# Kernel tuning notes

Measured on AMD Instinct MI355X. Metric: run time of the kernel, lower is better.

Reference implementation:

```python
import jax, jax.numpy as jnp
from jax import lax
import numpy as np

B, S, D = 64, 512, 256
VOCAB, NC = 50000, 10
N_STEPS = 10  # ode_step=11 points -> 10 intervals, h=0.1
BN_EPS = 1e-5


def setup_inputs() -> dict:
    key = jax.random.key(0)
    ks = jax.random.split(key, 16)
    inp = {}
    inp['input_ids'] = jax.random.randint(ks[0], (B, S), 0, VOCAB)
    inp['emb'] = jax.random.normal(ks[1], (VOCAB, D), dtype=jnp.float32)
    inp['W_ode'] = 0.1 * jax.random.normal(ks[2], (D, D), dtype=jnp.float32)  # init std=0.1
    inp['b_ode'] = jnp.zeros((D,), dtype=jnp.float32)
    for i, kk in enumerate([3, 4, 5]):
        fan_in = D * kk
        inp[f'w{kk}'] = jax.random.normal(ks[3 + 3 * i], (128, D, kk), jnp.float32) / np.sqrt(fan_in)
        inp[f'b{kk}'] = jax.random.normal(ks[4 + 3 * i], (128,), jnp.float32) * 0.01
        inp[f'g{kk}'] = jnp.ones((128,), jnp.float32)
        inp[f'be{kk}'] = jnp.zeros((128,), jnp.float32)
    inp['wc'] = jax.random.normal(ks[12], (NC, D + 3 * 128), jnp.float32) / np.sqrt(D + 3 * 128)
    inp['bc'] = jnp.zeros((NC,), jnp.float32)
    return inp


def _forward(input_ids, emb, W_ode, b_ode, w3, b3, g3, be3, w4, b4, g4, be4,
             w5, b5, g5, be5, wc, bc):
    x = emb[input_ids]                      # (B,S,D)
    # --- Neural ODE branch: linear RHS f(z) = z W^T + b, RK4 fixed-step on [0,1] ---
    z0 = x.reshape(-1, D)                   # (B*S, D)
    h = jnp.float32(1.0 / N_STEPS)

    def f(z):
        return z @ W_ode.T + b_ode

    def step(z, _):
        k1 = f(z)
        k2 = f(z + 0.5 * h * k1)
        k3 = f(z + 0.5 * h * k2)
        k4 = f(z + h * k3)
        return z + (h / 6.0) * (k1 + 2 * k2 + 2 * k3 + k4), None

    z, _ = lax.scan(step, z0, None, length=N_STEPS)
    node_pooled = z.reshape(B, S, D).max(axis=1)   # global max over seq -> (B,D)

    # --- TextCNN branches on raw embeddings ---
    cin = jnp.transpose(x, (0, 2, 1))       # (B,D,S)
    inv_std = jnp.float32(1.0 / np.sqrt(1.0 + BN_EPS))  # BN eval: mean=0, var=1

    def branch(w, b, g, be):
        c = lax.conv_general_dilated(cin, w, (1,), 'VALID',
                                     dimension_numbers=('NCH', 'OIH', 'NCH'))
        c = c + b[None, :, None]
        c = g[None, :, None] * (c * inv_std) + be[None, :, None]
        c = jax.nn.relu(c)
        return c.max(axis=2)                # (B,128)

    p3 = branch(w3, b3, g3, be3)
    p4 = branch(w4, b4, g4, be4)
    p5 = branch(w5, b5, g5, be5)

    feats = jnp.concatenate([node_pooled, p3, p4, p5], axis=1)  # (B,640)
    return feats @ wc.T + bc                # (B,NC); dropout is identity in eval


def reference(input_ids, emb, W_ode, b_ode, w3, b3, g3, be3, w4, b4, g4, be4,
              w5, b5, g5, be5, wc, bc):
    return _forward(input_ids, emb, W_ode, b_ode, w3, b3, g3, be3,
                    w4, b4, g4, be4, w5, b5, g5, be5, wc, bc)
```

## Files before the change

kernel.cpp:

```cpp
#include <hip/hip_runtime.h>


typedef short bf16x8 __attribute__((ext_vector_type(8)));
typedef float f32x4 __attribute__((ext_vector_type(4)));

__device__ __forceinline__ unsigned short f2bf(float f) {
  unsigned u = __float_as_uint(f);
  u += 0x7FFFu + ((u >> 16) & 1u);
  return (unsigned short)(u >> 16);
}

__device__ __forceinline__ float dotcol64(const float* __restrict__ xrow,
                                          const float* __restrict__ Y, int c) {
  float a0 = 0.f, a1 = 0.f, a2 = 0.f, a3 = 0.f;
#pragma unroll 1
  for (int w = 0; w < 4; ++w) {
    float bv[64];
#pragma unroll
    for (int v = 0; v < 64; ++v) bv[v] = Y[(w * 64 + v) * 256 + c];
#pragma unroll
    for (int v = 0; v < 64; v += 4) {
      a0 = fmaf(xrow[w * 64 + v + 0], bv[v + 0], a0);
      a1 = fmaf(xrow[w * 64 + v + 1], bv[v + 1], a1);
      a2 = fmaf(xrow[w * 64 + v + 2], bv[v + 2], a2);
      a3 = fmaf(xrow[w * 64 + v + 3], bv[v + 3], a3);
    }
  }
  return (a0 + a1) + (a2 + a3);
}

__global__ __launch_bounds__(256) void k_prep1(
    const float* __restrict__ W, const float* __restrict__ bode,
    const float* __restrict__ w3c, const float* __restrict__ w4c, const float* __restrict__ w5c,
    float* __restrict__ Bm, float* __restrict__ c1,
    unsigned short* __restrict__ slab, unsigned* __restrict__ featbuf) {
  __shared__ float r1[256], r2[256], r3[256], red[4];
  const int tid = threadIdx.x, blk = blockIdx.x;
  if (blk < 256) {
    const int i = blk;
    r1[tid] = W[i * 256 + tid];
    __syncthreads();
    const float v2 = dotcol64(r1, W, tid);
    r2[tid] = v2;
    __syncthreads();
    const float v3 = dotcol64(r2, W, tid);
    r3[tid] = v3;
    __syncthreads();
    const float v4 = dotcol64(r3, W, tid);
    const float w1 = r1[tid];
    Bm[i * 256 + tid] = 0.1f * w1 + 0.005f * v2
                      + (0.001f / 6.f) * v3 + (0.0001f / 24.f) * v4;
    const float q = 0.05f * w1 + (0.01f / 6.f) * v2 + (0.001f / 24.f) * v3;
    float val = bode[tid] * q;
#pragma unroll
    for (int off = 32; off > 0; off >>= 1) val += __shfl_down(val, off);
    if ((tid & 63) == 0) red[tid >> 6] = val;
    __syncthreads();
    if (tid == 0) c1[i] = 0.1f * (bode[i] + ((red[0] + red[1]) + (red[2] + red[3])));
  } else {
    const int base = (blk - 256) * 256 + tid;
#pragma unroll
    for (int u = 0; u < 4; ++u) {
      int e = base + u * 98304;
      int s = e >> 15, r = e & 32767;
      int o = r >> 8, kd = r & 255;
      const float* w; int k, j;
      if (s < 3)      { w = w3c; k = 3; j = s; }
      else if (s < 7) { w = w4c; k = 4; j = s - 3; }
      else            { w = w5c; k = 5; j = s - 7; }
      float val = w[(o * 256 + kd) * k + j];
      int kc = kd >> 5, quad = (kd >> 3) & 3, q8 = kd & 7;
      slab[s * 32768 + ((kc * 4 + quad) * 128 + o) * 8 + q8] = f2bf(val);
    }
    if (base < 64 * 640) featbuf[base] = 0u;
  }
}

__global__ __launch_bounds__(256) void k_prep2a(
    const float* __restrict__ Bm, const float* __restrict__ c1v,
    float* __restrict__ Dm, float* __restrict__ c1b) {
  __shared__ float r1[256], c1s[256], red[4];
  const int tid = threadIdx.x, i = blockIdx.x;
  r1[tid] = Bm[i * 256 + tid];
  c1s[tid] = c1v[tid];
  __syncthreads();
  const float v2 = dotcol64(r1, Bm, tid);
  Dm[i * 256 + tid] = 2.f * r1[tid] + v2;
  float pd = r1[tid] * c1s[tid];
#pragma unroll
  for (int off = 32; off > 0; off >>= 1) pd += __shfl_down(pd, off);
  if ((tid & 63) == 0) red[tid >> 6] = pd;
  __syncthreads();
  if (tid == 0) c1b[i] = 2.f * c1s[i] + ((red[0] + red[1]) + (red[2] + red[3]));
}

__global__ __launch_bounds__(256) void k_prep2b(
    const float* __restrict__ Dm, const float* __restrict__ c1bv,
    float* __restrict__ c10, unsigned short* __restrict__ slab) {
  __shared__ float curs[256], cbs[256], red[4];
  const int tid = threadIdx.x, i = blockIdx.x;
  const float coefN[6] = {1.f, 5.f, 10.f, 10.f, 5.f, 1.f};
  const float coefC[5] = {5.f, 10.f, 10.f, 5.f, 1.f};
  float v = Dm[i * 256 + tid];
  curs[tid] = v;
  cbs[tid] = c1bv[tid];
  __syncthreads();
  float n10 = ((i == tid) ? 1.f : 0.f) + coefN[1] * v;
  float pd = v * cbs[tid];
#pragma unroll
  for (int off = 32; off > 0; off >>= 1) pd += __shfl_down(pd, off);
  if ((tid & 63) == 0) red[tid >> 6] = pd;
  __syncthreads();
  float ct = coefC[0] * cbs[i] + coefC[1] * ((red[0] + red[1]) + (red[2] + red[3]));

#pragma unroll 1
  for (int k = 2; k <= 5; ++k) {
    v = dotcol64(curs, Dm, tid);
    __syncthreads();
    curs[tid] = v;
    n10 = fmaf(coefN[k], v, n10);
    float pdk = v * cbs[tid];
#pragma unroll
    for (int off = 32; off > 0; off >>= 1) pdk += __shfl_down(pdk, off);
    if ((tid & 63) == 0) red[tid >> 6] = pdk;
    __syncthreads();
    if (k <= 4) ct = fmaf(coefC[k], (red[0] + red[1]) + (red[2] + red[3]), ct);
  }

  {
    const int o = i, kd = tid;
    const int kc = kd >> 5, quad = (kd >> 3) & 3, q8 = kd & 7;
    slab[(12 + (o >> 7)) * 32768 + ((kc * 4 + quad) * 128 + (o & 127)) * 8 + q8] = f2bf(n10);
  }
  if (tid == 0) c10[i] = ct;
}


__global__ __launch_bounds__(256, 4) void k_main(
    const int* __restrict__ ids, const float* __restrict__ emb,
    const unsigned short* __restrict__ slab, const float* __restrict__ ctot,
    const float* __restrict__ b3, const float* __restrict__ g3, const float* __restrict__ be3,
    const float* __restrict__ b4, const float* __restrict__ g4, const float* __restrict__ be4,
    const float* __restrict__ b5, const float* __restrict__ g5, const float* __restrict__ be5,
    unsigned* __restrict__ featbuf) {
  __shared__ alignas(16) unsigned short Xt[36 * 264];
  __shared__ int ids_s[36];
  const int tid = threadIdx.x;
  const int blk = blockIdx.x;
  const int b = blk & 63;
  const int t0 = (blk >> 6) * 32;
  const int lane = tid & 63;
  const int wave = tid >> 6;
  const int m15 = lane & 15;
  const int quad = lane >> 4;

  if (tid < 36) {
    int t = t0 + tid;
    ids_s[tid] = (t < 512) ? ids[b * 512 + t] : -1;
  }
  __syncthreads();
  for (int i = tid; i < 36 * 64; i += 256) {
    int row = i >> 6, s4 = i & 63;
    uint2 v = make_uint2(0u, 0u);
    int id = ids_s[row];
    if (id >= 0) {
      const float4 f = *(const float4*)(emb + (size_t)id * 256 + s4 * 4);
      v.x = (unsigned)f2bf(f.x) | ((unsigned)f2bf(f.y) << 16);
      v.y = (unsigned)f2bf(f.z) | ((unsigned)f2bf(f.w) << 16);
    }
    *(uint2*)&Xt[row * 264 + s4 * 4] = v;
  }
  __syncthreads();

  const unsigned short* fb0 = slab + ((size_t)quad * 128 + (wave * 2 + 0) * 16 + m15) * 8;
  const unsigned short* fb1 = fb0 + 128;

  bf16x8 fA[4], fB[4];
#pragma unroll
  for (int q = 0; q < 4; ++q) {
    fA[q] = *(const bf16x8*)(((q & 1) ? fb1 : fb0) + (q >> 1) * 4096);
    fB[q] = *(const bf16x8*)(((q & 1) ? fb1 : fb0) + 8192 + (q >> 1) * 4096);
  }

  f32x4 acc[2][2];
#pragma unroll
  for (int mt = 0; mt < 2; ++mt)
#pragma unroll
    for (int nt = 0; nt < 2; ++nt) acc[mt][nt] = (f32x4){0.f, 0.f, 0.f, 0.f};

#define ENTRY(KCQ, FR)                                                          \
  {                                                                             \
    __builtin_amdgcn_s_setprio(1);                                              \
    _Pragma("unroll")                                                           \
    for (int kc2 = 0; kc2 < 2; ++kc2) {                                         \
      const int kd0 = ((KCQ) * 2 + kc2) * 32 + quad * 8;                        \
      bf16x8 af[2];                                                             \
      _Pragma("unroll")                                                         \
      for (int mt = 0; mt < 2; ++mt)                                            \
        af[mt] = *(const bf16x8*)&Xt[(shift + mt * 16 + m15) * 264 + kd0];      \
      _Pragma("unroll")                                                         \
      for (int mt = 0; mt < 2; ++mt) {                                          \
        acc[mt][0] = __builtin_amdgcn_mfma_f32_16x16x32_bf16(af[mt], FR[kc2 * 2 + 0], acc[mt][0], 0, 0, 0); \
        acc[mt][1] = __builtin_amdgcn_mfma_f32_16x16x32_bf16(af[mt], FR[kc2 * 2 + 1], acc[mt][1], 0, 0, 0); \
      }                                                                         \
    }                                                                           \
    __builtin_amdgcn_s_setprio(0);                                              \
  }

  for (int ep = 0; ep < 28; ++ep) {
    const int e0 = ep * 2;
    const int slice = e0 >> 2;
    const int shift = (slice < 3) ? slice
                    : (slice < 7) ? (slice - 3)
                    : (slice < 12) ? (slice - 7) : 0;
    const int kcq0 = e0 & 3;

    ENTRY(kcq0, fA);
    if (ep < 27) {
      const int eo = (e0 + 2) * 8192;
#pragma unroll
      for (int q = 0; q < 4; ++q)
        fA[q] = *(const bf16x8*)(((q & 1) ? fb1 : fb0) + eo + (q >> 1) * 4096);
    }
    ENTRY(kcq0 + 1, fB);
    if (ep < 27) {
      const int eo = (e0 + 3) * 8192;
#pragma unroll
      for (int q = 0; q < 4; ++q)
        fB[q] = *(const bf16x8*)(((q & 1) ? fb1 : fb0) + eo + (q >> 1) * 4096);
    }

    const int g = (ep == 5) ? 0 : (ep == 13) ? 1 : (ep == 23) ? 2
                : (ep == 25) ? 3 : (ep == 27) ? 4 : -1;
    if (g >= 0) {
      if (g < 3) {
        const int kk = g + 3;
        const float* bb  = (g == 0) ? b3 : (g == 1) ? b4 : b5;
        const float* gg  = (g == 0) ? g3 : (g == 1) ? g4 : g5;
        const float* bbe = (g == 0) ? be3 : (g == 1) ? be4 : be5;
        const int off = 256 + g * 128;
        const int tmax = 512 - kk;
#pragma unroll
        for (int nt = 0; nt < 2; ++nt) {
          const int n = (wave * 2 + nt) * 16 + m15;
          const float sc = gg[n] * 0.9999950000375f;
          const float sh = fmaf(sc, bb[n], bbe[n]);
          float mx = 0.f;
#pragma unroll
          for (int mt = 0; mt < 2; ++mt)
#pragma unroll
            for (int r = 0; r < 4; ++r) {
              const int t = t0 + mt * 16 + quad * 4 + r;
              const float v = fmaf(sc, acc[mt][nt][r], sh);
              if (t <= tmax) mx = fmaxf(mx, v);
            }
          mx = fmaxf(mx, __shfl_xor(mx, 16));
          mx = fmaxf(mx, __shfl_xor(mx, 32));
          if (quad == 0) atomicMax(&featbuf[b * 640 + off + n], __float_as_uint(mx));
        }
      } else {
        const int base = (g == 3) ? 0 : 128;
#pragma unroll
        for (int nt = 0; nt < 2; ++nt) {
          const int n = (wave * 2 + nt) * 16 + m15;
          const float ct = ctot[base + n];
          float mx = -3.4e38f;
#pragma unroll
          for (int mt = 0; mt < 2; ++mt)
#pragma unroll
            for (int r = 0; r < 4; ++r)
              mx = fmaxf(mx, acc[mt][nt][r] + ct);
          mx = fmaxf(mx, __shfl_xor(mx, 16));
          mx = fmaxf(mx, __shfl_xor(mx, 32));
          if (quad == 0) {
            unsigned bits = __float_as_uint(mx);
            unsigned key = (bits & 0x80000000u) ? ~bits : (bits | 0x80000000u);
            atomicMax(&featbuf[b * 640 + base + n], key);
          }
        }
      }
#pragma unroll
      for (int mt = 0; mt < 2; ++mt)
#pragma unroll
        for (int nt = 0; nt < 2; ++nt) acc[mt][nt] = (f32x4){0.f, 0.f, 0.f, 0.f};
    }
  }
#undef ENTRY
}

__global__ void k_fin(const unsigned* __restrict__ featbuf, const float* __restrict__ wc,
                      const float* __restrict__ bc, float* __restrict__ out) {
  int b = blockIdx.x, lane = threadIdx.x;
  float p[10];
#pragma unroll
  for (int c = 0; c < 10; ++c) p[c] = 0.f;
  for (int f = lane; f < 640; f += 64) {
    unsigned u = featbuf[b * 640 + f];
    float v;
    if (f < 256) v = (u & 0x80000000u) ? __uint_as_float(u ^ 0x80000000u) : __uint_as_float(~u);
    else v = __uint_as_float(u);
#pragma unroll
    for (int c = 0; c < 10; ++c) p[c] = fmaf(v, wc[c * 640 + f], p[c]);
  }
#pragma unroll
  for (int c = 0; c < 10; ++c) {
    float s = p[c];
#pragma unroll
    for (int off = 32; off > 0; off >>= 1) s += __shfl_down(s, off);
    if (lane == 0) out[b * 10 + c] = s + bc[c];
  }
}

extern "C" void kernel_launch(void* const* d_in, const int* in_sizes, int n_in,
                              void* d_out, int out_size, void* d_ws, size_t ws_size,
                              hipStream_t stream) {
  (void)in_sizes; (void)n_in; (void)out_size; (void)ws_size;
  const int*   ids  = (const int*)d_in[0];
  const float* emb  = (const float*)d_in[1];
  const float* W    = (const float*)d_in[2];
  const float* bode = (const float*)d_in[3];
  const float* w3   = (const float*)d_in[4];
  const float* b3   = (const float*)d_in[5];
  const float* g3   = (const float*)d_in[6];
  const float* be3  = (const float*)d_in[7];
  const float* w4   = (const float*)d_in[8];
  const float* b4   = (const float*)d_in[9];
  const float* g4   = (const float*)d_in[10];
  const float* be4  = (const float*)d_in[11];
  const float* w5   = (const float*)d_in[12];
  const float* b5   = (const float*)d_in[13];
  const float* g5   = (const float*)d_in[14];
  const float* be5  = (const float*)d_in[15];
  const float* wc   = (const float*)d_in[16];
  const float* bc   = (const float*)d_in[17];
  float* out = (float*)d_out;

  float* wsf = (float*)d_ws;
  float* Bm  = wsf;
  float* Dm  = wsf + 65536;
  float* c1  = wsf + 131072;
  float* c1b = wsf + 131328;
  float* c10 = wsf + 131584;
  unsigned short* slab = (unsigned short*)(wsf + 131840);
  unsigned* featbuf = (unsigned*)(wsf + 361216);

  hipLaunchKernelGGL(k_prep1, dim3(640), dim3(256), 0, stream,
                     W, bode, w3, w4, w5, Bm, c1, slab, featbuf);
  hipLaunchKernelGGL(k_prep2a, dim3(256), dim3(256), 0, stream, Bm, c1, Dm, c1b);
  hipLaunchKernelGGL(k_prep2b, dim3(256), dim3(256), 0, stream, Dm, c1b, c10, slab);
  hipLaunchKernelGGL(k_main, dim3(1024), dim3(256), 0, stream,
                     ids, emb, slab, c10,
                     b3, g3, be3, b4, g4, be4, b5, g5, be5, featbuf);
  hipLaunchKernelGGL(k_fin, dim3(64), dim3(64), 0, stream, featbuf, wc, bc, out);
}
```

Measured before the change: 202.7 us.

## Fuse ODE matrix-power prep into main kernel with flag-based overlap

The k_prep2b kernel is folded into k_main. The first 256 blocks compute the RK4 propagator power and bias, store them with agent-scope atomics, and bump a completion counter. The conv blocks wait on that counter only before the ODE slabs at epoch 23, so the prep work overlaps the conv work and one launch is removed. Each main block now covers 64 timesteps instead of 32, which halves the block count and doubles accumulator tiles per wave, and setprio is dropped. The spin-wait relies on the producer blocks being scheduled first; if they are not, the kernel can deadlock. The larger tiles also raise register and LDS pressure.

```diff
diff --git a/kernel.cpp b/kernel.cpp
--- a/kernel.cpp
+++ b/kernel.cpp
@@ -8,6 +8,13 @@
   unsigned u = __float_as_uint(f);
   u += 0x7FFFu + ((u >> 16) & 1u);
   return (unsigned short)(u >> 16);
+}
+
+__device__ __forceinline__ void gstf(float* p, float v) {
+  __hip_atomic_store(p, v, __ATOMIC_RELAXED, __HIP_MEMORY_SCOPE_AGENT);
+}
+__device__ __forceinline__ void gst16(unsigned short* p, unsigned short v) {
+  __hip_atomic_store(p, v, __ATOMIC_RELAXED, __HIP_MEMORY_SCOPE_AGENT);
 }
 
 __device__ __forceinline__ float dotcol64(const float* __restrict__ xrow,
@@ -72,7 +79,7 @@
       int kc = kd >> 5, quad = (kd >> 3) & 3, q8 = kd & 7;
       slab[s * 32768 + ((kc * 4 + quad) * 128 + o) * 8 + q8] = f2bf(val);
     }
-    if (base < 64 * 640) featbuf[base] = 0u;
+    if (base <= 64 * 640) featbuf[base] = 0u;
   }
 }
 
@@ -94,72 +101,81 @@
   if (tid == 0) c1b[i] = 2.f * c1s[i] + ((red[0] + red[1]) + (red[2] + red[3]));
 }
 
-__global__ __launch_bounds__(256) void k_prep2b(
-    const float* __restrict__ Dm, const float* __restrict__ c1bv,
-    float* __restrict__ c10, unsigned short* __restrict__ slab) {
-  __shared__ float curs[256], cbs[256], red[4];
-  const int tid = threadIdx.x, i = blockIdx.x;
-  const float coefN[6] = {1.f, 5.f, 10.f, 10.f, 5.f, 1.f};
-  const float coefC[5] = {5.f, 10.f, 10.f, 5.f, 1.f};
-  float v = Dm[i * 256 + tid];
-  curs[tid] = v;
-  cbs[tid] = c1bv[tid];
-  __syncthreads();
-  float n10 = ((i == tid) ? 1.f : 0.f) + coefN[1] * v;
-  float pd = v * cbs[tid];
-#pragma unroll
-  for (int off = 32; off > 0; off >>= 1) pd += __shfl_down(pd, off);
-  if ((tid & 63) == 0) red[tid >> 6] = pd;
-  __syncthreads();
-  float ct = coefC[0] * cbs[i] + coefC[1] * ((red[0] + red[1]) + (red[2] + red[3]));
-
-#pragma unroll 1
-  for (int k = 2; k <= 5; ++k) {
-    v = dotcol64(curs, Dm, tid);
-    __syncthreads();
-    curs[tid] = v;
-    n10 = fmaf(coefN[k], v, n10);
-    float pdk = v * cbs[tid];
-#pragma unroll
-    for (int off = 32; off > 0; off >>= 1) pdk += __shfl_down(pdk, off);
-    if ((tid & 63) == 0) red[tid >> 6] = pdk;
-    __syncthreads();
-    if (k <= 4) ct = fmaf(coefC[k], (red[0] + red[1]) + (red[2] + red[3]), ct);
-  }
-
-  {
-    const int o = i, kd = tid;
-    const int kc = kd >> 5, quad = (kd >> 3) & 3, q8 = kd & 7;
-    slab[(12 + (o >> 7)) * 32768 + ((kc * 4 + quad) * 128 + (o & 127)) * 8 + q8] = f2bf(n10);
-  }
-  if (tid == 0) c10[i] = ct;
-}
-
 
 __global__ __launch_bounds__(256, 4) void k_main(
     const int* __restrict__ ids, const float* __restrict__ emb,
-    const unsigned short* __restrict__ slab, const float* __restrict__ ctot,
+    unsigned short* __restrict__ slab, const float* __restrict__ Dm,
+    const float* __restrict__ c1bv, float* __restrict__ c10,
     const float* __restrict__ b3, const float* __restrict__ g3, const float* __restrict__ be3,
     const float* __restrict__ b4, const float* __restrict__ g4, const float* __restrict__ be4,
     const float* __restrict__ b5, const float* __restrict__ g5, const float* __restrict__ be5,
     unsigned* __restrict__ featbuf) {
-  __shared__ alignas(16) unsigned short Xt[36 * 264];
-  __shared__ int ids_s[36];
+  __shared__ alignas(16) unsigned short Xt[68 * 264];
+  __shared__ int ids_s[68];
   const int tid = threadIdx.x;
   const int blk = blockIdx.x;
-  const int b = blk & 63;
-  const int t0 = (blk >> 6) * 32;
+  unsigned* nodecnt = featbuf + 64 * 640;
+
+  if (blk < 256) {
+    float* curs = (float*)Xt;
+    float* cbs  = curs + 256;
+    float* redp = curs + 512;
+    const int i = blk;
+    const float coefN[6] = {1.f, 5.f, 10.f, 10.f, 5.f, 1.f};
+    const float coefC[5] = {5.f, 10.f, 10.f, 5.f, 1.f};
+    float v = Dm[i * 256 + tid];
+    curs[tid] = v;
+    cbs[tid] = c1bv[tid];
+    __syncthreads();
+    float n10 = ((i == tid) ? 1.f : 0.f) + coefN[1] * v;
+    float pd = v * cbs[tid];
+#pragma unroll
+    for (int off = 32; off > 0; off >>= 1) pd += __shfl_down(pd, off);
+    if ((tid & 63) == 0) redp[tid >> 6] = pd;
+    __syncthreads();
+    float ct = coefC[0] * cbs[i] + coefC[1] * ((redp[0] + redp[1]) + (redp[2] + redp[3]));
+
+#pragma unroll 1
+    for (int k = 2; k <= 5; ++k) {
+      v = dotcol64(curs, Dm, tid);
+      __syncthreads();
+      curs[tid] = v;
+      n10 = fmaf(coefN[k], v, n10);
+      float pdk = v * cbs[tid];
+#pragma unroll
+      for (int off = 32; off > 0; off >>= 1) pdk += __shfl_down(pdk, off);
+      if ((tid & 63) == 0) redp[tid >> 6] = pdk;
+      __syncthreads();
+      if (k <= 4) ct = fmaf(coefC[k], (redp[0] + redp[1]) + (redp[2] + redp[3]), ct);
+    }
+
+    {
+      const int o = i, kd = tid;
+      const int kc = kd >> 5, quad = (kd >> 3) & 3, q8 = kd & 7;
+      gst16(&slab[(12 + (o >> 7)) * 32768 + ((kc * 4 + quad) * 128 + (o & 127)) * 8 + q8],
+            f2bf(n10));
+    }
+    if (tid == 0) gstf(&c10[i], ct);
+    __syncthreads();
+    if (tid == 0)
+      __hip_atomic_fetch_add(nodecnt, 1u, __ATOMIC_RELEASE, __HIP_MEMORY_SCOPE_AGENT);
+    return;
+  }
+
+  const int mb = blk - 256;
+  const int b = mb >> 3;
+  const int t0 = (mb & 7) * 64;
   const int lane = tid & 63;
   const int wave = tid >> 6;
   const int m15 = lane & 15;
   const int quad = lane >> 4;
 
-  if (tid < 36) {
+  if (tid < 68) {
     int t = t0 + tid;
     ids_s[tid] = (t < 512) ? ids[b * 512 + t] : -1;
   }
   __syncthreads();
-  for (int i = tid; i < 36 * 64; i += 256) {
+  for (int i = tid; i < 68 * 64; i += 256) {
     int row = i >> 6, s4 = i & 63;
     uint2 v = make_uint2(0u, 0u);
     int id = ids_s[row];
@@ -182,32 +198,37 @@
     fB[q] = *(const bf16x8*)(((q & 1) ? fb1 : fb0) + 8192 + (q >> 1) * 4096);
   }
 
-  f32x4 acc[2][2];
-#pragma unroll
-  for (int mt = 0; mt < 2; ++mt)
+  f32x4 acc[4][2];
+#pragma unroll
+  for (int mt = 0; mt < 4; ++mt)
 #pragma unroll
     for (int nt = 0; nt < 2; ++nt) acc[mt][nt] = (f32x4){0.f, 0.f, 0.f, 0.f};
 
 #define ENTRY(KCQ, FR)                                                          \
   {                                                                             \
-    __builtin_amdgcn_s_setprio(1);                                              \
     _Pragma("unroll")                                                           \
     for (int kc2 = 0; kc2 < 2; ++kc2) {                                         \
       const int kd0 = ((KCQ) * 2 + kc2) * 32 + quad * 8;                        \
-      bf16x8 af[2];                                                             \
+      bf16x8 af[4];                                                             \
       _Pragma("unroll")                                                         \
-      for (int mt = 0; mt < 2; ++mt)                                            \
+      for (int mt = 0; mt < 4; ++mt)                                            \
         af[mt] = *(const bf16x8*)&Xt[(shift + mt * 16 + m15) * 264 + kd0];      \
       _Pragma("unroll")                                                         \
-      for (int mt = 0; mt < 2; ++mt) {                                          \
+      for (int mt = 0; mt < 4; ++mt) {                                          \
         acc[mt][0] = __builtin_amdgcn_mfma_f32_16x16x32_bf16(af[mt], FR[kc2 * 2 + 0], acc[mt][0], 0, 0, 0); \
         acc[mt][1] = __builtin_amdgcn_mfma_f32_16x16x32_bf16(af[mt], FR[kc2 * 2 + 1], acc[mt][1], 0, 0, 0); \
       }                                                                         \
     }                                                                           \
-    __builtin_amdgcn_s_setprio(0);                                              \
   }
 
   for (int ep = 0; ep < 28; ++ep) {
+    if (ep == 23) {
+      if (tid == 0) {
+        while (__hip_atomic_load(nodecnt, __ATOMIC_ACQUIRE, __HIP_MEMORY_SCOPE_AGENT) < 256u)
+          __builtin_amdgcn_s_sleep(8);
+      }
+      __syncthreads();
+    }
     const int e0 = ep * 2;
     const int slice = e0 >> 2;
     const int shift = (slice < 3) ? slice
@@ -247,7 +268,7 @@
           const float sh = fmaf(sc, bb[n], bbe[n]);
           float mx = 0.f;
 #pragma unroll
-          for (int mt = 0; mt < 2; ++mt)
+          for (int mt = 0; mt < 4; ++mt)
 #pragma unroll
             for (int r = 0; r < 4; ++r) {
               const int t = t0 + mt * 16 + quad * 4 + r;
@@ -263,10 +284,10 @@
 #pragma unroll
         for (int nt = 0; nt < 2; ++nt) {
           const int n = (wave * 2 + nt) * 16 + m15;
-          const float ct = ctot[base + n];
+          const float ct = c10[base + n];
           float mx = -3.4e38f;
 #pragma unroll
-          for (int mt = 0; mt < 2; ++mt)
+          for (int mt = 0; mt < 4; ++mt)
 #pragma unroll
             for (int r = 0; r < 4; ++r)
               mx = fmaxf(mx, acc[mt][nt][r] + ct);
@@ -280,7 +301,7 @@
         }
       }
 #pragma unroll
-      for (int mt = 0; mt < 2; ++mt)
+      for (int mt = 0; mt < 4; ++mt)
 #pragma unroll
         for (int nt = 0; nt < 2; ++nt) acc[mt][nt] = (f32x4){0.f, 0.f, 0.f, 0.f};
     }
@@ -347,9 +368,8 @@
   hipLaunchKernelGGL(k_prep1, dim3(640), dim3(256), 0, stream,
                      W, bode, w3, w4, w5, Bm, c1, slab, featbuf);
   hipLaunchKernelGGL(k_prep2a, dim3(256), dim3(256), 0, stream, Bm, c1, Dm, c1b);
-  hipLaunchKernelGGL(k_prep2b, dim3(256), dim3(256), 0, stream, Dm, c1b, c10, slab);
-  hipLaunchKernelGGL(k_main, dim3(1024), dim3(256), 0, stream,
-                     ids, emb, slab, c10,
+  hipLaunchKernelGGL(k_main, dim3(768), dim3(256), 0, stream,
+                     ids, emb, slab, Dm, c1b, c10,
                      b3, g3, be3, b4, g4, be4, b5, g5, be5, featbuf);
   hipLaunchKernelGGL(k_fin, dim3(64), dim3(64), 0, stream, featbuf, wc, bc, out);
 }
```

After: 188.5 us. 1.08x faster.
